# Performance work log

Measured on AMD Instinct MI355X. Metric: run time of the kernel, lower is better.

## Reference

```python
import jax, jax.numpy as jnp
import numpy as np

N = 50_000
E = 800_000
H = 128
EDGE_DIM = 1
NEG = 0.01  # leaky_relu slope used throughout AttentiveFP


def _lrelu(x):
    return jnp.where(x >= 0, x, NEG * x)


def _seg_softmax(logits, seg, num_segments):
    # numerically stable softmax over edges grouped by target segment
    m = jax.ops.segment_max(logits, seg, num_segments=num_segments)
    e = jnp.exp(logits - m[seg])
    s = jax.ops.segment_sum(e, seg, num_segments=num_segments)
    return e / s[seg]


def _gru(x, h, Wih, Whh, bih, bhh):
    # torch.nn.GRUCell: gates ordered r, z, n
    gi = x @ Wih.T + bih
    gh = h @ Whh.T + bhh
    ir, iz, inn = jnp.split(gi, 3, axis=-1)
    hr, hz, hn = jnp.split(gh, 3, axis=-1)
    r = jax.nn.sigmoid(ir + hr)
    z = jax.nn.sigmoid(iz + hz)
    n = jnp.tanh(inn + r * hn)
    return (1.0 - z) * n + z * h


def setup_inputs() -> dict:
    key = jax.random.key(0)
    ks = jax.random.split(key, 32)
    def rn(k, shape, s=0.1):
        return jax.random.normal(k, shape, dtype=jnp.float32) * s
    return {
        "node_attr": jax.random.normal(ks[0], (N, 1), dtype=jnp.float32),
        "edge_index": jax.random.randint(ks[1], (2, E), 0, N),
        "edge_attr": jax.random.normal(ks[2], (E, EDGE_DIM), dtype=jnp.float32),
        "W_lin1": rn(ks[3], (H, 1)), "b_lin1": rn(ks[4], (H,)),
        "gate_W1": rn(ks[5], (H, H + EDGE_DIM)), "gate_W2": rn(ks[6], (H, H)),
        "gate_att_l": rn(ks[7], (H,)), "gate_att_r": rn(ks[8], (H,)),
        "gate_b": rn(ks[9], (H,)),
        "gru1_Wih": rn(ks[10], (3 * H, H)), "gru1_Whh": rn(ks[11], (3 * H, H)),
        "gru1_bih": rn(ks[12], (3 * H,)), "gru1_bhh": rn(ks[13], (3 * H,)),
        "atom_W": rn(ks[14], (H, H)), "atom_att_src": rn(ks[15], (H,)),
        "atom_att_dst": rn(ks[16], (H,)), "atom_b": rn(ks[17], (H,)),
        "gru2_Wih": rn(ks[18], (3 * H, H)), "gru2_Whh": rn(ks[19], (3 * H, H)),
        "gru2_bih": rn(ks[20], (3 * H,)), "gru2_bhh": rn(ks[21], (3 * H,)),
        "mol_W": rn(ks[22], (H, H)), "mol_att_src": rn(ks[23], (H,)),
        "mol_att_dst": rn(ks[24], (H,)), "mol_b": rn(ks[25], (H,)),
        "grum_Wih": rn(ks[26], (3 * H, H)), "grum_Whh": rn(ks[27], (3 * H, H)),
        "grum_bih": rn(ks[28], (3 * H,)), "grum_bhh": rn(ks[29], (3 * H,)),
    }


def _forward(node_attr, edge_index, edge_attr, W_lin1, b_lin1, gate_W1, gate_W2,
             gate_att_l, gate_att_r, gate_b, gru1_Wih, gru1_Whh, gru1_bih, gru1_bhh,
             atom_W, atom_att_src, atom_att_dst, atom_b, gru2_Wih, gru2_Whh,
             gru2_bih, gru2_bhh, mol_W, mol_att_src, mol_att_dst, mol_b,
             grum_Wih, grum_Whh, grum_bih, grum_bhh):
    src, dst = edge_index[0], edge_index[1]  # j -> i (aggregate at dst)
    n = node_attr.shape[0]
    # lin1 + leaky_relu
    x = _lrelu(node_attr @ W_lin1.T + b_lin1)  # [N,H]
    # --- GATEConv (edge-featured attention) ---
    xj = _lrelu(jnp.concatenate([x[src], edge_attr], axis=-1) @ gate_W1.T)  # [E,H]
    alpha = _lrelu(xj @ gate_att_l + (x @ gate_att_r)[dst])  # [E]
    alpha = _seg_softmax(alpha, dst, n)
    h = jax.ops.segment_sum((x[src] @ gate_W2.T) * alpha[:, None], dst, num_segments=n) + gate_b
    h = jax.nn.elu(h)
    x = jax.nn.relu(_gru(h, x, gru1_Wih, gru1_Whh, gru1_bih, gru1_bhh))
    # --- GATConv layer (num_layers=2 -> one) ---
    xt = x @ atom_W.T  # [N,H]
    a = _lrelu((xt * atom_att_src).sum(-1)[src] + (xt * atom_att_dst).sum(-1)[dst])
    a = _seg_softmax(a, dst, n)
    h = jax.ops.segment_sum(xt[src] * a[:, None], dst, num_segments=n) + atom_b
    h = jax.nn.elu(h)
    x = jax.nn.relu(_gru(h, x, gru2_Wih, gru2_Whh, gru2_bih, gru2_bhh))
    # --- molecule embedding: batch = zeros -> single graph; num_timesteps=1 ---
    batch = jnp.zeros((n,), dtype=jnp.int32)
    out = jax.nn.relu(jax.ops.segment_sum(x, batch, num_segments=1))  # [1,H]
    xs = x @ mol_W.T          # node-side transform (shared lin)
    outs = out @ mol_W.T      # graph-side transform
    a = _lrelu((xs * mol_att_src).sum(-1) + (outs * mol_att_dst).sum(-1)[batch])
    a = _seg_softmax(a, batch, 1)
    h = jax.nn.elu(jax.ops.segment_sum(xs * a[:, None], batch, num_segments=1) + mol_b)
    out = jax.nn.relu(_gru(h, out, grum_Wih, grum_Whh, grum_bih, grum_bhh))
    return out  # [1, H] graph embedding (layer1 output, out_channels=hidden)


def reference(node_attr, edge_index, edge_attr, W_lin1, b_lin1, gate_W1, gate_W2,
              gate_att_l, gate_att_r, gate_b, gru1_Wih, gru1_Whh, gru1_bih, gru1_bhh,
              atom_W, atom_att_src, atom_att_dst, atom_b, gru2_Wih, gru2_Whh,
              gru2_bih, gru2_bhh, mol_W, mol_att_src, mol_att_dst, mol_b,
              grum_Wih, grum_Whh, grum_bih, grum_bhh):
    return _forward(node_attr, edge_index, edge_attr, W_lin1, b_lin1, gate_W1,
                    gate_W2, gate_att_l, gate_att_r, gate_b, gru1_Wih, gru1_Whh,
                    gru1_bih, gru1_bhh, atom_W, atom_att_src, atom_att_dst, atom_b,
                    gru2_Wih, gru2_Whh, gru2_bih, gru2_bhh, mol_W, mol_att_src,
                    mol_att_dst, mol_b, grum_Wih, grum_Whh, grum_bih, grum_bhh)
```

## Files before the change

### kernel.cpp

```cpp
#include <hip/hip_runtime.h>
#include <math.h>

#define H 128
#define NEGS 0.01f

typedef __attribute__((ext_vector_type(8))) short short8;
typedef __attribute__((ext_vector_type(4))) float f32x4;

__device__ __forceinline__ float lrelu(float x){ return x >= 0.f ? x : NEGS*x; }
__device__ __forceinline__ float eluf(float x){ return x > 0.f ? x : expf(x)-1.f; }
__device__ __forceinline__ float sigm(float x){ return 1.f/(1.f+expf(-x)); }
__device__ __forceinline__ float wred(float v){
  #pragma unroll
  for (int off = 32; off > 0; off >>= 1) v += __shfl_xor(v, off, 64);
  return v;
}
__device__ __forceinline__ float wredmax(float v){
  #pragma unroll
  for (int off = 32; off > 0; off >>= 1) v = fmaxf(v, __shfl_xor(v, off, 64));
  return v;
}
__device__ __forceinline__ unsigned fenc(float f){
  unsigned u = __float_as_uint(f);
  return (u & 0x80000000u) ? ~u : (u | 0x80000000u);
}
__device__ __forceinline__ float fdec(unsigned v){
  return __uint_as_float((v & 0x80000000u) ? (v ^ 0x80000000u) : ~v);
}
__device__ __forceinline__ unsigned short f2bf(float f){
  unsigned u = __float_as_uint(f);
  u += 0x7fffu + ((u >> 16) & 1u);
  return (unsigned short)(u >> 16);
}
__device__ __forceinline__ float bf2f(unsigned short h){
  return __uint_as_float(((unsigned)h) << 16);
}
__device__ __forceinline__ float rdlane(float v, int l){
  return __int_as_float(__builtin_amdgcn_readlane(__float_as_int(v), l));
}
__device__ __forceinline__ int rdlanei(int v, int l){
  return __builtin_amdgcn_readlane(v, l);
}

#define SMS 140

__global__ void k_castall(const float* __restrict__ gW1, const float* __restrict__ gW2,
                          const float* __restrict__ atomW, const float* __restrict__ molW,
                          const float* __restrict__ g1ih, const float* __restrict__ g1hh,
                          const float* __restrict__ g2ih, const float* __restrict__ g2hh,
                          unsigned short* __restrict__ dst){
  int idx = blockIdx.x*256 + threadIdx.x;
  const float* src; int ld = 128; int off;
  if      (idx <  16384){ src = gW1;  ld = 129; off = idx; }
  else if (idx <  32768){ src = gW2;  off = idx -  16384; }
  else if (idx <  49152){ src = atomW;off = idx -  32768; }
  else if (idx <  65536){ src = molW; off = idx -  49152; }
  else if (idx < 114688){ src = g1ih; off = idx -  65536; }
  else if (idx < 163840){ src = g1hh; off = idx - 114688; }
  else if (idx < 212992){ src = g2ih; off = idx - 163840; }
  else                  { src = g2hh; off = idx - 212992; }
  int r = off >> 7, c = off & 127;
  dst[idx] = f2bf(src[r*ld + c]);
}

__global__ void k_node_init_rd(const float* __restrict__ na, const float* __restrict__ wl,
                               const float* __restrict__ bl, const float* __restrict__ attr,
                               unsigned short* __restrict__ x, float* __restrict__ rdot, int n){
  int i = blockIdx.x*4 + (threadIdx.x >> 6);
  int lane = threadIdx.x & 63;
  if (i >= n) return;
  float nav = na[i];
  float v0 = lrelu(nav*wl[2*lane]   + bl[2*lane]);
  float v1 = lrelu(nav*wl[2*lane+1] + bl[2*lane+1]);
  ushort2 o; o.x = f2bf(v0); o.y = f2bf(v1);
  *(ushort2*)&x[(size_t)i*H + 2*lane] = o;
  float d = bf2f(o.x)*attr[2*lane] + bf2f(o.y)*attr[2*lane+1];
  d = wred(d);
  if (lane == 0) rdot[i] = d;
}

__global__ __launch_bounds__(256)
void k_gemm_mfma(const unsigned short* __restrict__ X, const unsigned short* __restrict__ Wbf,
                 unsigned short* __restrict__ Y, int n, int ldy, size_t ostride,
                 const float* __restrict__ v1, const float* __restrict__ v2,
                 float* __restrict__ o1, float* __restrict__ o2){
  __shared__ unsigned short sm[128*SMS];
  int w = threadIdx.x >> 6;
  int l = threadIdx.x & 63;
  int nb = blockIdx.x*128;
  int mbase = blockIdx.y*128;
  int row = l & 15;
  int kg  = l >> 4;
  f32x4 acc[2][8];
  #pragma unroll
  for (int f = 0; f < 2; ++f)
    #pragma unroll
    for (int c = 0; c < 8; ++c) acc[f][c] = (f32x4){0.f,0.f,0.f,0.f};
  int a0 = nb + w*16 + row;
  int a1 = nb + 64 + w*16 + row;
  bool v0 = (a0 < n), v1ok = (a1 < n);
  #pragma unroll
  for (int ks = 0; ks < 4; ++ks){
    int koff = ks*32 + kg*8;
    short8 A0 = v0  ? *(const short8*)&X[(size_t)a0*H + koff] : (short8){0,0,0,0,0,0,0,0};
    short8 A1 = v1ok? *(const short8*)&X[(size_t)a1*H + koff] : (short8){0,0,0,0,0,0,0,0};
    #pragma unroll
    for (int c = 0; c < 8; ++c){
      short8 b = *(const short8*)&Wbf[(size_t)(mbase + c*16 + row)*H + koff];
      acc[0][c] = __builtin_amdgcn_mfma_f32_16x16x32_bf16(A0, b, acc[0][c], 0, 0, 0);
      acc[1][c] = __builtin_amdgcn_mfma_f32_16x16x32_bf16(A1, b, acc[1][c], 0, 0, 0);
    }
  }
  #pragma unroll
  for (int f = 0; f < 2; ++f)
    #pragma unroll
    for (int c = 0; c < 8; ++c)
      #pragma unroll
      for (int r = 0; r < 4; ++r){
        int nl = f*64 + w*16 + kg*4 + r;
        sm[nl*SMS + c*16 + row] = f2bf(acc[f][c][r]);
      }
  if (v1){
    #pragma unroll
    for (int f = 0; f < 2; ++f)
      #pragma unroll
      for (int r = 0; r < 4; ++r){
        float p1 = 0.f, p2 = 0.f;
        #pragma unroll
        for (int c = 0; c < 8; ++c){
          p1 += acc[f][c][r]*v1[c*16 + row];
          if (v2) p2 += acc[f][c][r]*v2[c*16 + row];
        }
        #pragma unroll
        for (int off = 1; off < 16; off <<= 1){
          p1 += __shfl_xor(p1, off, 64);
          if (v2) p2 += __shfl_xor(p2, off, 64);
        }
        int i = nb + f*64 + w*16 + kg*4 + r;
        if (row == 0 && i < n){ o1[i] = p1; if (v2) o2[i] = p2; }
      }
  }
  __syncthreads();
  unsigned short* Yb = Y + (size_t)blockIdx.y*ostride;
  int t = threadIdx.x;
  #pragma unroll
  for (int p = 0; p < 16; ++p){
    int nl = p*8 + (t >> 5);
    int c4 = (t & 31)*4;
    int i = nb + nl;
    if (i < n) *(ushort4*)&Yb[(size_t)i*ldy + c4] = *(const ushort4*)&sm[nl*SMS + c4];
  }
}

__global__ __launch_bounds__(256)
void k_gemm_gru(const unsigned short* __restrict__ Xi, const unsigned short* __restrict__ Xh,
                const unsigned short* __restrict__ Wbf, unsigned short* __restrict__ gi,
                unsigned short* __restrict__ gh, int n){
  __shared__ unsigned short sm[128*SMS];
  int w = threadIdx.x >> 6;
  int l = threadIdx.x & 63;
  int nb = blockIdx.x*256;
  int y = blockIdx.y;
  const unsigned short* X = (y < 3) ? Xi : Xh;
  unsigned short* Y = (y < 3) ? gi : gh;
  int mbase = y*128;
  int cbase = (y < 3 ? y : y-3)*128;
  int row = l & 15;
  int kg  = l >> 4;
  f32x4 acc[4][8];
  #pragma unroll
  for (int f = 0; f < 4; ++f)
    #pragma unroll
    for (int c = 0; c < 8; ++c) acc[f][c] = (f32x4){0.f,0.f,0.f,0.f};
  int ai[4]; bool av[4];
  #pragma unroll
  for (int f = 0; f < 4; ++f){
    ai[f] = nb + f*64 + w*16 + row;
    av[f] = (ai[f] < n);
  }
  #pragma unroll
  for (int ks = 0; ks < 4; ++ks){
    int koff = ks*32 + kg*8;
    short8 A[4];
    #pragma unroll
    for (int f = 0; f < 4; ++f)
      A[f] = av[f] ? *(const short8*)&X[(size_t)ai[f]*H + koff] : (short8){0,0,0,0,0,0,0,0};
    #pragma unroll
    for (int c = 0; c < 8; ++c){
      short8 b = *(const short8*)&Wbf[(size_t)(mbase + c*16 + row)*H + koff];
      acc[0][c] = __builtin_amdgcn_mfma_f32_16x16x32_bf16(A[0], b, acc[0][c], 0, 0, 0);
      acc[1][c] = __builtin_amdgcn_mfma_f32_16x16x32_bf16(A[1], b, acc[1][c], 0, 0, 0);
      acc[2][c] = __builtin_amdgcn_mfma_f32_16x16x32_bf16(A[2], b, acc[2][c], 0, 0, 0);
      acc[3][c] = __builtin_amdgcn_mfma_f32_16x16x32_bf16(A[3], b, acc[3][c], 0, 0, 0);
    }
  }
  int t = threadIdx.x;
  #pragma unroll
  for (int half = 0; half < 2; ++half){
    if (half) __syncthreads();
    #pragma unroll
    for (int ff = 0; ff < 2; ++ff){
      int f = half*2 + ff;
      #pragma unroll
      for (int c = 0; c < 8; ++c)
        #pragma unroll
        for (int r = 0; r < 4; ++r){
          int nl = ff*64 + w*16 + kg*4 + r;
          sm[nl*SMS + c*16 + row] = f2bf(acc[f][c][r]);
        }
    }
    __syncthreads();
    #pragma unroll
    for (int p = 0; p < 16; ++p){
      int nl = p*8 + (t >> 5);
      int c4 = (t & 31)*4;
      int i = nb + half*128 + nl;
      if (i < n) *(ushort4*)&Y[(size_t)i*384 + cbase + c4] = *(const ushort4*)&sm[nl*SMS + c4];
    }
  }
}

__global__ void k_gru_combine(const unsigned short* __restrict__ gi, const unsigned short* __restrict__ gh,
                              const float* __restrict__ bih, const float* __restrict__ bhh,
                              unsigned short* __restrict__ x, int n){
  int idx = blockIdx.x*blockDim.x + threadIdx.x;
  if (idx >= n*64) return;
  int i = idx >> 6, t = (idx & 63)*2;
  const unsigned short* gir = gi + (size_t)i*384;
  const unsigned short* ghr = gh + (size_t)i*384;
  ushort2 uir = *(const ushort2*)&gir[t];
  ushort2 uiz = *(const ushort2*)&gir[t+128];
  ushort2 uin = *(const ushort2*)&gir[t+256];
  ushort2 uhr = *(const ushort2*)&ghr[t];
  ushort2 uhz = *(const ushort2*)&ghr[t+128];
  ushort2 uhn = *(const ushort2*)&ghr[t+256];
  ushort2 ux  = *(const ushort2*)&x[(size_t)i*H + t];
  float2 b_ir = *(const float2*)&bih[t], b_iz = *(const float2*)&bih[t+128], b_in = *(const float2*)&bih[t+256];
  float2 b_hr = *(const float2*)&bhh[t], b_hz = *(const float2*)&bhh[t+128], b_hn = *(const float2*)&bhh[t+256];
  ushort2 o;
  {
    float r = sigm(bf2f(uir.x)+b_ir.x + bf2f(uhr.x)+b_hr.x);
    float z = sigm(bf2f(uiz.x)+b_iz.x + bf2f(uhz.x)+b_hz.x);
    float nn = tanhf(bf2f(uin.x)+b_in.x + r*(bf2f(uhn.x)+b_hn.x));
    o.x = f2bf(fmaxf((1.f-z)*nn + z*bf2f(ux.x), 0.f));
  }
  {
    float r = sigm(bf2f(uir.y)+b_ir.y + bf2f(uhr.y)+b_hr.y);
    float z = sigm(bf2f(uiz.y)+b_iz.y + bf2f(uhz.y)+b_hz.y);
    float nn = tanhf(bf2f(uin.y)+b_in.y + r*(bf2f(uhn.y)+b_hn.y));
    o.y = f2bf(fmaxf((1.f-z)*nn + z*bf2f(ux.y), 0.f));
  }
  *(ushort2*)&x[(size_t)i*H + t] = o;
}

__global__ void k_hist(const int* __restrict__ key, int* __restrict__ deg, int ne){
  int e = blockIdx.x*blockDim.x + threadIdx.x;
  if (e < ne) atomicAdd(&deg[key[e]], 1);
}
__global__ void k_scan1(const int* __restrict__ deg, int* __restrict__ bsum, int n){
  __shared__ int sd[256];
  int i = blockIdx.x*256 + threadIdx.x;
  sd[threadIdx.x] = (i < n) ? deg[i] : 0;
  __syncthreads();
  for (int s = 128; s > 0; s >>= 1){
    if (threadIdx.x < s) sd[threadIdx.x] += sd[threadIdx.x+s];
    __syncthreads();
  }
  if (threadIdx.x == 0) bsum[blockIdx.x] = sd[0];
}
__global__ void k_scan2(int* __restrict__ bsum, int nb){
  __shared__ int sd[256];
  int t = threadIdx.x;
  int v = (t < nb) ? bsum[t] : 0;
  sd[t] = v;
  __syncthreads();
  for (int off = 1; off < 256; off <<= 1){
    int u = (t >= off) ? sd[t-off] : 0;
    __syncthreads();
    sd[t] += u;
    __syncthreads();
  }
  if (t < nb) bsum[t] = sd[t] - v;
}
__global__ void k_scan3(const int* __restrict__ deg, const int* __restrict__ boff,
                        int* __restrict__ rowptr, int* __restrict__ cursor, int n){
  __shared__ int sd[256];
  int t = threadIdx.x;
  int i = blockIdx.x*256 + t;
  int v = (i < n) ? deg[i] : 0;
  sd[t] = v;
  __syncthreads();
  for (int off = 1; off < 256; off <<= 1){
    int u = (t >= off) ? sd[t-off] : 0;
    __syncthreads();
    sd[t] += u;
    __syncthreads();
  }
  int excl = sd[t] - v + boff[blockIdx.x];
  if (i < n){
    rowptr[i] = excl; cursor[i] = excl;
    if (i == n-1) rowptr[n] = excl + v;
  }
}
__global__ void k_fill_dst(const int* __restrict__ src, const int* __restrict__ dst,
                           const float* __restrict__ ea, int* __restrict__ cursor,
                           int2* __restrict__ sea, int ne){
  int e = blockIdx.x*blockDim.x + threadIdx.x;
  if (e >= ne) return;
  int pos = atomicAdd(&cursor[dst[e]], 1);
  sea[pos] = make_int2(src[e], __float_as_int(ea[e]));
}

__global__ void k_pack_gate(const float* __restrict__ gateW1, float* __restrict__ w1col){
  int t = threadIdx.x;
  if (t < H) w1col[t] = gateW1[t*129 + 128];
}

__global__ __launch_bounds__(256)
void k_edge_logit_gate(const unsigned short* __restrict__ xW1, const float* __restrict__ w1col,
                       const float* __restrict__ attl, const int2* __restrict__ sea,
                       float* __restrict__ logit_s, int ne){
  int tid = threadIdx.x;
  int j = blockIdx.x*32 + (tid >> 3);
  int g = tid & 7;
  if (j >= ne) return;
  int2 se = sea[j];
  int s = se.x;
  float eav = __int_as_float(se.y);
  const unsigned short* xr = &xW1[(size_t)s*H + g*16];
  short8 r0 = *(const short8*)xr;
  short8 r1 = *(const short8*)(xr + 8);
  float acc = 0.f;
  #pragma unroll
  for (int kk = 0; kk < 8; ++kk)
    acc += lrelu(bf2f((unsigned short)r0[kk]) + eav*w1col[g*16 + kk]) * attl[g*16 + kk];
  #pragma unroll
  for (int kk = 0; kk < 8; ++kk)
    acc += lrelu(bf2f((unsigned short)r1[kk]) + eav*w1col[g*16 + 8 + kk]) * attl[g*16 + 8 + kk];
  #pragma unroll
  for (int off = 1; off < 8; off <<= 1) acc += __shfl_xor(acc, off, 64);
  if (g == 0) logit_s[j] = acc;
}

__global__ void k_node_agg(const int* __restrict__ rowptr, const int2* __restrict__ sea,
                           const float* __restrict__ logit_s, const float* __restrict__ rdot,
                           const unsigned short* __restrict__ val, const float* __restrict__ bias,
                           unsigned short* __restrict__ hbuf, int n){
  int i = blockIdx.x*4 + (threadIdx.x >> 6);
  int lane = threadIdx.x & 63;
  if (i >= n) return;
  int b = rowptr[i], e1 = rowptr[i+1];
  float rd = rdot[i];
  float m = -1e30f;
  for (int j = b+lane; j < e1; j += 64) m = fmaxf(m, lrelu(logit_s[j] + rd));
  m = wredmax(m);
  float s = 0.f, ax = 0.f, ay = 0.f;
  for (int c0 = b; c0 < e1; c0 += 64){
    int cnt = min(64, e1 - c0);
    float wv = 0.f; int snv = 0;
    if (lane < cnt){
      snv = sea[c0 + lane].x;
      wv = expf(lrelu(logit_s[c0 + lane] + rd) - m);
    }
    s += wred(wv);
    int j = 0;
    for (; j+8 <= cnt; j += 8){
      #pragma unroll
      for (int u = 0; u < 8; ++u){
        float wq = rdlane(wv, j+u);
        int sq = rdlanei(snv, j+u);
        ushort2 v = *(const ushort2*)&val[(size_t)sq*H + 2*lane];
        ax += bf2f(v.x)*wq; ay += bf2f(v.y)*wq;
      }
    }
    for (; j < cnt; ++j){
      float wq = rdlane(wv, j);
      int sq = rdlanei(snv, j);
      ushort2 v = *(const ushort2*)&val[(size_t)sq*H + 2*lane];
      ax += bf2f(v.x)*wq; ay += bf2f(v.y)*wq;
    }
  }
  float inv = (s > 0.f) ? 1.f/s : 0.f;
  ushort2 o;
  o.x = f2bf(eluf(bias[2*lane]   + ax*inv));
  o.y = f2bf(eluf(bias[2*lane+1] + ay*inv));
  *(ushort2*)&hbuf[(size_t)i*H + 2*lane] = o;
}

__global__ void k_node_agg_gat(const int* __restrict__ rowptr, const int2* __restrict__ sea,
                               const float* __restrict__ ssrc, const float* __restrict__ sdst,
                               const unsigned short* __restrict__ val, const float* __restrict__ bias,
                               unsigned short* __restrict__ hbuf, int n){
  int i = blockIdx.x*4 + (threadIdx.x >> 6);
  int lane = threadIdx.x & 63;
  if (i >= n) return;
  int b = rowptr[i], e1 = rowptr[i+1];
  float sdi = sdst[i];
  float m = -1e30f;
  for (int j = b+lane; j < e1; j += 64) m = fmaxf(m, lrelu(ssrc[sea[j].x] + sdi));
  m = wredmax(m);
  float s = 0.f, ax = 0.f, ay = 0.f;
  for (int c0 = b; c0 < e1; c0 += 64){
    int cnt = min(64, e1 - c0);
    float wv = 0.f; int snv = 0;
    if (lane < cnt){
      snv = sea[c0 + lane].x;
      wv = expf(lrelu(ssrc[snv] + sdi) - m);
    }
    s += wred(wv);
    int j = 0;
    for (; j+8 <= cnt; j += 8){
      #pragma unroll
      for (int u = 0; u < 8; ++u){
        float wq = rdlane(wv, j+u);
        int sq = rdlanei(snv, j+u);
        ushort2 v = *(const ushort2*)&val[(size_t)sq*H + 2*lane];
        ax += bf2f(v.x)*wq; ay += bf2f(v.y)*wq;
      }
    }
    for (; j < cnt; ++j){
      float wq = rdlane(wv, j);
      int sq = rdlanei(snv, j);
      ushort2 v = *(const ushort2*)&val[(size_t)sq*H + 2*lane];
      ax += bf2f(v.x)*wq; ay += bf2f(v.y)*wq;
    }
  }
  float inv = (s > 0.f) ? 1.f/s : 0.f;
  ushort2 o;
  o.x = f2bf(eluf(bias[2*lane]   + ax*inv));
  o.y = f2bf(eluf(bias[2*lane+1] + ay*inv));
  *(ushort2*)&hbuf[(size_t)i*H + 2*lane] = o;
}

__global__ void k_colsum(const unsigned short* __restrict__ x, float* __restrict__ outraw,
                         int n, int chunk){
  int t = threadIdx.x;
  int start = blockIdx.x*chunk;
  int end = min(start + chunk, n);
  float s0 = 0.f, s1 = 0.f;
  for (int i = start; i < end; ++i){
    ushort2 v = *(const ushort2*)&x[(size_t)i*H + 2*t];
    s0 += bf2f(v.x); s1 += bf2f(v.y);
  }
  if (start < end){ atomicAdd(&outraw[2*t], s0); atomicAdd(&outraw[2*t+1], s1); }
}
__global__ void k_mol_prep(const float* __restrict__ outraw, const float* __restrict__ molW,
                           const float* __restrict__ attdst, float* __restrict__ hidvec,
                           float* __restrict__ cdst){
  __shared__ float hs[128];
  __shared__ float red[128];
  int t = threadIdx.x;
  float hv = fmaxf(outraw[t], 0.f);
  hs[t] = hv; hidvec[t] = hv;
  __syncthreads();
  float o = 0.f;
  for (int k = 0; k < 128; ++k) o += hs[k]*molW[t*128+k];
  red[t] = o * attdst[t];
  __syncthreads();
  for (int s = 64; s > 0; s >>= 1){
    if (t < s) red[t] += red[t+s];
    __syncthreads();
  }
  if (t == 0) cdst[0] = red[0];
}
__global__ void k_mol_logit(float* __restrict__ a, const float* __restrict__ cdst,
                            unsigned* __restrict__ gmax, int n){
  int i = blockIdx.x*blockDim.x + threadIdx.x;
  int lane = threadIdx.x & 63;
  float l = -1e30f;
  if (i < n){
    l = lrelu(a[i] + cdst[0]);
    a[i] = l;
  }
  float mm = wredmax(l);
  if (lane == 0) atomicMax(gmax, fenc(mm));
}
__global__ void k_mol_exp(float* __restrict__ a, const unsigned* __restrict__ gmax,
                          float* __restrict__ gsum, int n){
  int i = blockIdx.x*blockDim.x + threadIdx.x;
  int lane = threadIdx.x & 63;
  float gm = fdec(gmax[0]);
  float ex = 0.f;
  if (i < n){ ex = expf(a[i] - gm); a[i] = ex; }
  float s = wred(ex);
  if (lane == 0) atomicAdd(gsum, s);
}
__global__ void k_mol_acc(const unsigned short* __restrict__ xs, const float* __restrict__ a,
                          float* __restrict__ num, int n, int chunk){
  int t = threadIdx.x;
  int start = blockIdx.x*chunk;
  int end = min(start + chunk, n);
  float s0 = 0.f, s1 = 0.f;
  for (int i = start; i < end; ++i){
    float ai = a[i];
    ushort2 v = *(const ushort2*)&xs[(size_t)i*H + 2*t];
    s0 += bf2f(v.x)*ai; s1 += bf2f(v.y)*ai;
  }
  if (start < end){ atomicAdd(&num[2*t], s0); atomicAdd(&num[2*t+1], s1); }
}
__global__ void k_mol_final(const float* __restrict__ num, const float* __restrict__ gsum,
                            const float* __restrict__ molb, const float* __restrict__ hidvec,
                            const float* __restrict__ Wih, const float* __restrict__ Whh,
                            const float* __restrict__ bih, const float* __restrict__ bhh,
                            float* __restrict__ out){
  __shared__ float hv[128], hd[128];
  int t = threadIdx.x;
  hv[t] = eluf(num[t]/gsum[0] + molb[t]);
  hd[t] = hidvec[t];
  __syncthreads();
  float gr = bih[t], gz = bih[t+128], gn = bih[t+256];
  float hr = bhh[t], hz = bhh[t+128], hn = bhh[t+256];
  for (int k = 0; k < 128; ++k){
    float h = hv[k], d = hd[k];
    gr += h*Wih[t*128+k];       gz += h*Wih[(t+128)*128+k]; gn += h*Wih[(t+256)*128+k];
    hr += d*Whh[t*128+k];       hz += d*Whh[(t+128)*128+k]; hn += d*Whh[(t+256)*128+k];
  }
  float r = sigm(gr+hr), z = sigm(gz+hz);
  float nn = tanhf(gn + r*hn);
  float o = (1.f-z)*nn + z*hd[t];
  out[t] = fmaxf(o, 0.f);
}

extern "C" void kernel_launch(void* const* d_in, const int* in_sizes, int n_in,
                              void* d_out, int out_size, void* d_ws, size_t ws_size,
                              hipStream_t stream){
  const float* node_attr = (const float*)d_in[0];
  const int*   eidx      = (const int*)d_in[1];
  const float* eattr     = (const float*)d_in[2];
  const float* W_lin1    = (const float*)d_in[3];
  const float* b_lin1    = (const float*)d_in[4];
  const float* gate_W1   = (const float*)d_in[5];
  const float* gate_W2   = (const float*)d_in[6];
  const float* gate_att_l= (const float*)d_in[7];
  const float* gate_att_r= (const float*)d_in[8];
  const float* gate_b    = (const float*)d_in[9];
  const float* g1_Wih    = (const float*)d_in[10];
  const float* g1_Whh    = (const float*)d_in[11];
  const float* g1_bih    = (const float*)d_in[12];
  const float* g1_bhh    = (const float*)d_in[13];
  const float* atom_W    = (const float*)d_in[14];
  const float* atom_as   = (const float*)d_in[15];
  const float* atom_ad   = (const float*)d_in[16];
  const float* atom_b    = (const float*)d_in[17];
  const float* g2_Wih    = (const float*)d_in[18];
  const float* g2_Whh    = (const float*)d_in[19];
  const float* g2_bih    = (const float*)d_in[20];
  const float* g2_bhh    = (const float*)d_in[21];
  const float* mol_W     = (const float*)d_in[22];
  const float* mol_as    = (const float*)d_in[23];
  const float* mol_ad    = (const float*)d_in[24];
  const float* mol_b     = (const float*)d_in[25];
  const float* gm_Wih    = (const float*)d_in[26];
  const float* gm_Whh    = (const float*)d_in[27];
  const float* gm_bih    = (const float*)d_in[28];
  const float* gm_bhh    = (const float*)d_in[29];

  const int n  = in_sizes[0];
  const int ne = in_sizes[1] / 2;
  const int* src = eidx;
  const int* dst = eidx + ne;

  const size_t NH = (size_t)n * H;
  unsigned short* us = (unsigned short*)d_ws;
  unsigned short* x_bf = us;
  unsigned short* t0   = us + NH;
  unsigned short* t1   = us + 2*NH;
  unsigned short* hb   = us + 3*NH;
  unsigned short* gi   = us + 4*NH;
  unsigned short* gh   = us + 7*NH;
  float* fb = (float*)(us + 10*NH);
  float* rdot = fb;
  float* ssrc = rdot + n;
  float* sdst = ssrc + n;
  float* logit_s = sdst + n;
  int* deg    = (int*)(logit_s + ne);
  int* cursor = deg + n;
  int* rowptr = cursor + n;
  int* bsum   = rowptr + n + 1;
  size_t ioff = (size_t)(bsum + 256 - (int*)d_ws);
  ioff = (ioff + 1) & ~(size_t)1;
  int2* sea  = (int2*)((int*)d_ws + ioff);
  float* outraw = (float*)(sea + ne);
  float* hidvec = outraw + 128;
  float* cdstp  = hidvec + 128;
  unsigned* gmax = (unsigned*)(cdstp + 1);
  float* gsum   = (float*)gmax + 1;
  float* numv   = gsum + 1;
  float* w1col  = numv + 128 + 1;
  unsigned short* wp = (unsigned short*)(w1col + 128);
  unsigned short* gW1bf  = wp;
  unsigned short* gW2bf  = gW1bf  + 128*H;
  unsigned short* atomWbf= gW2bf  + 128*H;
  unsigned short* molWbf = atomWbf+ 128*H;
  unsigned short* g1ihbf = molWbf + 128*H;
  unsigned short* g1hhbf = g1ihbf + 384*H;
  unsigned short* g2ihbf = g1hhbf + 384*H;
  unsigned short* g2hhbf = g2ihbf + 384*H;

  const int nb128      = (n + 127)/128;
  const int nb256      = (n + 255)/256;
  const int nwave4     = (n + 3)/4;
  const int e32_blocks = (ne + 31)/32;
  const int ethr       = (ne + 255)/256;
  const int nthr       = (n + 255)/256;
  const int nb         = (n + 255)/256;
  const int chunk      = (n + 255)/256;
  const int gru_blocks = (n*64 + 255)/256;

  k_castall<<<1024,256,0,stream>>>(gate_W1, gate_W2, atom_W, mol_W,
                                   g1_Wih, g1_Whh, g2_Wih, g2_Whh, wp);
  k_pack_gate<<<1,128,0,stream>>>(gate_W1, w1col);
  k_node_init_rd<<<nwave4,256,0,stream>>>(node_attr, W_lin1, b_lin1, gate_att_r, x_bf, rdot, n);
  hipMemsetAsync(deg, 0, (size_t)n*4, stream);
  k_hist<<<ethr,256,0,stream>>>(dst, deg, ne);
  k_scan1<<<nb,256,0,stream>>>(deg, bsum, n);
  k_scan2<<<1,256,0,stream>>>(bsum, nb);
  k_scan3<<<nb,256,0,stream>>>(deg, bsum, rowptr, cursor, n);
  k_fill_dst<<<ethr,256,0,stream>>>(src, dst, eattr, cursor, sea, ne);

  k_gemm_mfma<<<dim3(nb128,2),256,0,stream>>>(x_bf, gW1bf, t0, n, H, NH,
                                              nullptr, nullptr, nullptr, nullptr);
  k_edge_logit_gate<<<e32_blocks,256,0,stream>>>(t0, w1col, gate_att_l, sea, logit_s, ne);
  k_node_agg<<<nwave4,256,0,stream>>>(rowptr, sea, logit_s, rdot, t1, gate_b, hb, n);
  k_gemm_gru<<<dim3(nb256,6),256,0,stream>>>(hb, x_bf, g1ihbf, gi, gh, n);
  k_gru_combine<<<gru_blocks,256,0,stream>>>(gi, gh, g1_bih, g1_bhh, x_bf, n);

  k_gemm_mfma<<<dim3(nb128,1),256,0,stream>>>(x_bf, atomWbf, t0, n, H, 0,
                                              atom_as, atom_ad, ssrc, sdst);
  k_node_agg_gat<<<nwave4,256,0,stream>>>(rowptr, sea, ssrc, sdst, t0, atom_b, hb, n);
  k_gemm_gru<<<dim3(nb256,6),256,0,stream>>>(hb, x_bf, g2ihbf, gi, gh, n);
  k_gru_combine<<<gru_blocks,256,0,stream>>>(gi, gh, g2_bih, g2_bhh, x_bf, n);

  hipMemsetAsync(outraw, 0, 128*4, stream);
  hipMemsetAsync(gmax, 0, 4, stream);
  hipMemsetAsync(gsum, 0, 4, stream);
  hipMemsetAsync(numv, 0, 128*4, stream);
  k_colsum<<<256,64,0,stream>>>(x_bf, outraw, n, chunk);
  k_mol_prep<<<1,128,0,stream>>>(outraw, mol_W, mol_ad, hidvec, cdstp);
  k_gemm_mfma<<<dim3(nb128,1),256,0,stream>>>(x_bf, molWbf, t1, n, H, 0,
                                              mol_as, nullptr, rdot, nullptr);
  k_mol_logit<<<nthr,256,0,stream>>>(rdot, cdstp, gmax, n);
  k_mol_exp<<<nthr,256,0,stream>>>(rdot, gmax, gsum, n);
  k_mol_acc<<<256,64,0,stream>>>(t1, rdot, numv, n, chunk);
  k_mol_final<<<1,128,0,stream>>>(numv, gsum, mol_b, hidvec,
                                  gm_Wih, gm_Whh, gm_bih, gm_bhh, (float*)d_out);
}
```

Before: 616.3 us.

## Widen GEMM row tile to 256 and split wave into half-waves in aggregation

The MFMA GEMM now processes 256 rows per block instead of 128, reusing each loaded weight fragment across four A fragments and staging output through shared memory in two halves. The node aggregation kernels now have each half-wave handle a different edge, loading 8 bytes per lane with shuffles in place of readlane, so two neighbour rows are gathered per iteration, and reduce the halves at the end. This aims to cut redundant weight loads in the GEMM and raise memory-level parallelism in the gather. The cost is higher register pressure from 128 accumulator floats per lane, half as many GEMM blocks, and an extra cross-half reduction.

```diff
diff --git a/kernel.cpp b/kernel.cpp
--- a/kernel.cpp
+++ b/kernel.cpp
@@ -34,12 +34,6 @@
 }
 __device__ __forceinline__ float bf2f(unsigned short h){
   return __uint_as_float(((unsigned)h) << 16);
-}
-__device__ __forceinline__ float rdlane(float v, int l){
-  return __int_as_float(__builtin_amdgcn_readlane(__float_as_int(v), l));
-}
-__device__ __forceinline__ int rdlanei(int v, int l){
-  return __builtin_amdgcn_readlane(v, l);
 }
 
 #define SMS 140
@@ -87,42 +81,40 @@
   __shared__ unsigned short sm[128*SMS];
   int w = threadIdx.x >> 6;
   int l = threadIdx.x & 63;
-  int nb = blockIdx.x*128;
+  int nb = blockIdx.x*256;
   int mbase = blockIdx.y*128;
   int row = l & 15;
   int kg  = l >> 4;
-  f32x4 acc[2][8];
-  #pragma unroll
-  for (int f = 0; f < 2; ++f)
+  f32x4 acc[4][8];
+  #pragma unroll
+  for (int f = 0; f < 4; ++f)
     #pragma unroll
     for (int c = 0; c < 8; ++c) acc[f][c] = (f32x4){0.f,0.f,0.f,0.f};
-  int a0 = nb + w*16 + row;
-  int a1 = nb + 64 + w*16 + row;
-  bool v0 = (a0 < n), v1ok = (a1 < n);
+  int ai[4]; bool av[4];
+  #pragma unroll
+  for (int f = 0; f < 4; ++f){
+    ai[f] = nb + f*64 + w*16 + row;
+    av[f] = (ai[f] < n);
+  }
   #pragma unroll
   for (int ks = 0; ks < 4; ++ks){
     int koff = ks*32 + kg*8;
-    short8 A0 = v0  ? *(const short8*)&X[(size_t)a0*H + koff] : (short8){0,0,0,0,0,0,0,0};
-    short8 A1 = v1ok? *(const short8*)&X[(size_t)a1*H + koff] : (short8){0,0,0,0,0,0,0,0};
+    short8 A[4];
+    #pragma unroll
+    for (int f = 0; f < 4; ++f)
+      A[f] = av[f] ? *(const short8*)&X[(size_t)ai[f]*H + koff] : (short8){0,0,0,0,0,0,0,0};
     #pragma unroll
     for (int c = 0; c < 8; ++c){
       short8 b = *(const short8*)&Wbf[(size_t)(mbase + c*16 + row)*H + koff];
-      acc[0][c] = __builtin_amdgcn_mfma_f32_16x16x32_bf16(A0, b, acc[0][c], 0, 0, 0);
-      acc[1][c] = __builtin_amdgcn_mfma_f32_16x16x32_bf16(A1, b, acc[1][c], 0, 0, 0);
-    }
-  }
-  #pragma unroll
-  for (int f = 0; f < 2; ++f)
-    #pragma unroll
-    for (int c = 0; c < 8; ++c)
-      #pragma unroll
-      for (int r = 0; r < 4; ++r){
-        int nl = f*64 + w*16 + kg*4 + r;
-        sm[nl*SMS + c*16 + row] = f2bf(acc[f][c][r]);
-      }
+      acc[0][c] = __builtin_amdgcn_mfma_f32_16x16x32_bf16(A[0], b, acc[0][c], 0, 0, 0);
+      acc[1][c] = __builtin_amdgcn_mfma_f32_16x16x32_bf16(A[1], b, acc[1][c], 0, 0, 0);
+      acc[2][c] = __builtin_amdgcn_mfma_f32_16x16x32_bf16(A[2], b, acc[2][c], 0, 0, 0);
+      acc[3][c] = __builtin_amdgcn_mfma_f32_16x16x32_bf16(A[3], b, acc[3][c], 0, 0, 0);
+    }
+  }
   if (v1){
     #pragma unroll
-    for (int f = 0; f < 2; ++f)
+    for (int f = 0; f < 4; ++f)
       #pragma unroll
       for (int r = 0; r < 4; ++r){
         float p1 = 0.f, p2 = 0.f;
@@ -140,15 +132,30 @@
         if (row == 0 && i < n){ o1[i] = p1; if (v2) o2[i] = p2; }
       }
   }
-  __syncthreads();
   unsigned short* Yb = Y + (size_t)blockIdx.y*ostride;
   int t = threadIdx.x;
   #pragma unroll
-  for (int p = 0; p < 16; ++p){
-    int nl = p*8 + (t >> 5);
-    int c4 = (t & 31)*4;
-    int i = nb + nl;
-    if (i < n) *(ushort4*)&Yb[(size_t)i*ldy + c4] = *(const ushort4*)&sm[nl*SMS + c4];
+  for (int half = 0; half < 2; ++half){
+    if (half) __syncthreads();
+    #pragma unroll
+    for (int ff = 0; ff < 2; ++ff){
+      int f = half*2 + ff;
+      #pragma unroll
+      for (int c = 0; c < 8; ++c)
+        #pragma unroll
+        for (int r = 0; r < 4; ++r){
+          int nl = ff*64 + w*16 + kg*4 + r;
+          sm[nl*SMS + c*16 + row] = f2bf(acc[f][c][r]);
+        }
+    }
+    __syncthreads();
+    #pragma unroll
+    for (int p = 0; p < 16; ++p){
+      int nl = p*8 + (t >> 5);
+      int c4 = (t & 31)*4;
+      int i = nb + half*128 + nl;
+      if (i < n) *(ushort4*)&Yb[(size_t)i*ldy + c4] = *(const ushort4*)&sm[nl*SMS + c4];
+    }
   }
 }
 
@@ -348,13 +355,16 @@
                            unsigned short* __restrict__ hbuf, int n){
   int i = blockIdx.x*4 + (threadIdx.x >> 6);
   int lane = threadIdx.x & 63;
+  int hl = lane >> 5;
+  int cl = lane & 31;
   if (i >= n) return;
   int b = rowptr[i], e1 = rowptr[i+1];
   float rd = rdot[i];
   float m = -1e30f;
   for (int j = b+lane; j < e1; j += 64) m = fmaxf(m, lrelu(logit_s[j] + rd));
   m = wredmax(m);
-  float s = 0.f, ax = 0.f, ay = 0.f;
+  float s = 0.f;
+  float a0=0.f, a1=0.f, a2=0.f, a3=0.f;
   for (int c0 = b; c0 < e1; c0 += 64){
     int cnt = min(64, e1 - c0);
     float wv = 0.f; int snv = 0;
@@ -364,27 +374,41 @@
     }
     s += wred(wv);
     int j = 0;
-    for (; j+8 <= cnt; j += 8){
+    for (; j+16 <= cnt; j += 16){
       #pragma unroll
       for (int u = 0; u < 8; ++u){
-        float wq = rdlane(wv, j+u);
-        int sq = rdlanei(snv, j+u);
-        ushort2 v = *(const ushort2*)&val[(size_t)sq*H + 2*lane];
-        ax += bf2f(v.x)*wq; ay += bf2f(v.y)*wq;
+        int jj = j + 2*u + hl;
+        float wq = __shfl(wv, jj, 64);
+        int sq = __shfl(snv, jj, 64);
+        ushort4 v = *(const ushort4*)&val[(size_t)sq*H + 4*cl];
+        a0 += bf2f(v.x)*wq; a1 += bf2f(v.y)*wq; a2 += bf2f(v.z)*wq; a3 += bf2f(v.w)*wq;
       }
     }
-    for (; j < cnt; ++j){
-      float wq = rdlane(wv, j);
-      int sq = rdlanei(snv, j);
-      ushort2 v = *(const ushort2*)&val[(size_t)sq*H + 2*lane];
-      ax += bf2f(v.x)*wq; ay += bf2f(v.y)*wq;
-    }
-  }
+    for (; j < cnt; j += 2){
+      int jj = j + hl;
+      int jjc = jj < 63 ? jj : 63;
+      float wq = __shfl(wv, jjc, 64);
+      int sq = __shfl(snv, jjc, 64);
+      if (jj < cnt){
+        ushort4 v = *(const ushort4*)&val[(size_t)sq*H + 4*cl];
+        a0 += bf2f(v.x)*wq; a1 += bf2f(v.y)*wq; a2 += bf2f(v.z)*wq; a3 += bf2f(v.w)*wq;
+      }
+    }
+  }
+  a0 += __shfl_xor(a0, 32, 64);
+  a1 += __shfl_xor(a1, 32, 64);
+  a2 += __shfl_xor(a2, 32, 64);
+  a3 += __shfl_xor(a3, 32, 64);
   float inv = (s > 0.f) ? 1.f/s : 0.f;
-  ushort2 o;
-  o.x = f2bf(eluf(bias[2*lane]   + ax*inv));
-  o.y = f2bf(eluf(bias[2*lane+1] + ay*inv));
-  *(ushort2*)&hbuf[(size_t)i*H + 2*lane] = o;
+  if (hl == 0){
+    float4 bb = *(const float4*)&bias[4*cl];
+    ushort4 o;
+    o.x = f2bf(eluf(bb.x + a0*inv));
+    o.y = f2bf(eluf(bb.y + a1*inv));
+    o.z = f2bf(eluf(bb.z + a2*inv));
+    o.w = f2bf(eluf(bb.w + a3*inv));
+    *(ushort4*)&hbuf[(size_t)i*H + 4*cl] = o;
+  }
 }
 
 __global__ void k_node_agg_gat(const int* __restrict__ rowptr, const int2* __restrict__ sea,
@@ -393,13 +417,16 @@
                                unsigned short* __restrict__ hbuf, int n){
   int i = blockIdx.x*4 + (threadIdx.x >> 6);
   int lane = threadIdx.x & 63;
+  int hl = lane >> 5;
+  int cl = lane & 31;
   if (i >= n) return;
   int b = rowptr[i], e1 = rowptr[i+1];
   float sdi = sdst[i];
   float m = -1e30f;
   for (int j = b+lane; j < e1; j += 64) m = fmaxf(m, lrelu(ssrc[sea[j].x] + sdi));
   m = wredmax(m);
-  float s = 0.f, ax = 0.f, ay = 0.f;
+  float s = 0.f;
+  float a0=0.f, a1=0.f, a2=0.f, a3=0.f;
   for (int c0 = b; c0 < e1; c0 += 64){
     int cnt = min(64, e1 - c0);
     float wv = 0.f; int snv = 0;
@@ -409,27 +436,41 @@
     }
     s += wred(wv);
     int j = 0;
-    for (; j+8 <= cnt; j += 8){
+    for (; j+16 <= cnt; j += 16){
       #pragma unroll
       for (int u = 0; u < 8; ++u){
-        float wq = rdlane(wv, j+u);
-        int sq = rdlanei(snv, j+u);
-        ushort2 v = *(const ushort2*)&val[(size_t)sq*H + 2*lane];
-        ax += bf2f(v.x)*wq; ay += bf2f(v.y)*wq;
+        int jj = j + 2*u + hl;
+        float wq = __shfl(wv, jj, 64);
+        int sq = __shfl(snv, jj, 64);
+        ushort4 v = *(const ushort4*)&val[(size_t)sq*H + 4*cl];
+        a0 += bf2f(v.x)*wq; a1 += bf2f(v.y)*wq; a2 += bf2f(v.z)*wq; a3 += bf2f(v.w)*wq;
       }
     }
-    for (; j < cnt; ++j){
-      float wq = rdlane(wv, j);
-      int sq = rdlanei(snv, j);
-      ushort2 v = *(const ushort2*)&val[(size_t)sq*H + 2*lane];
-      ax += bf2f(v.x)*wq; ay += bf2f(v.y)*wq;
-    }
-  }
+    for (; j < cnt; j += 2){
+      int jj = j + hl;
+      int jjc = jj < 63 ? jj : 63;
+      float wq = __shfl(wv, jjc, 64);
+      int sq = __shfl(snv, jjc, 64);
+      if (jj < cnt){
+        ushort4 v = *(const ushort4*)&val[(size_t)sq*H + 4*cl];
+        a0 += bf2f(v.x)*wq; a1 += bf2f(v.y)*wq; a2 += bf2f(v.z)*wq; a3 += bf2f(v.w)*wq;
+      }
+    }
+  }
+  a0 += __shfl_xor(a0, 32, 64);
+  a1 += __shfl_xor(a1, 32, 64);
+  a2 += __shfl_xor(a2, 32, 64);
+  a3 += __shfl_xor(a3, 32, 64);
   float inv = (s > 0.f) ? 1.f/s : 0.f;
-  ushort2 o;
-  o.x = f2bf(eluf(bias[2*lane]   + ax*inv));
-  o.y = f2bf(eluf(bias[2*lane+1] + ay*inv));
-  *(ushort2*)&hbuf[(size_t)i*H + 2*lane] = o;
+  if (hl == 0){
+    float4 bb = *(const float4*)&bias[4*cl];
+    ushort4 o;
+    o.x = f2bf(eluf(bb.x + a0*inv));
+    o.y = f2bf(eluf(bb.y + a1*inv));
+    o.z = f2bf(eluf(bb.z + a2*inv));
+    o.w = f2bf(eluf(bb.w + a3*inv));
+    *(ushort4*)&hbuf[(size_t)i*H + 4*cl] = o;
+  }
 }
 
 __global__ void k_colsum(const unsigned short* __restrict__ x, float* __restrict__ outraw,
@@ -597,7 +638,6 @@
   unsigned short* g2ihbf = g1hhbf + 384*H;
   unsigned short* g2hhbf = g2ihbf + 384*H;
 
-  const int nb128      = (n + 127)/128;
   const int nb256      = (n + 255)/256;
   const int nwave4     = (n + 3)/4;
   const int e32_blocks = (ne + 31)/32;
@@ -618,14 +658,14 @@
   k_scan3<<<nb,256,0,stream>>>(deg, bsum, rowptr, cursor, n);
   k_fill_dst<<<ethr,256,0,stream>>>(src, dst, eattr, cursor, sea, ne);
 
-  k_gemm_mfma<<<dim3(nb128,2),256,0,stream>>>(x_bf, gW1bf, t0, n, H, NH,
+  k_gemm_mfma<<<dim3(nb256,2),256,0,stream>>>(x_bf, gW1bf, t0, n, H, NH,
                                               nullptr, nullptr, nullptr, nullptr);
   k_edge_logit_gate<<<e32_blocks,256,0,stream>>>(t0, w1col, gate_att_l, sea, logit_s, ne);
   k_node_agg<<<nwave4,256,0,stream>>>(rowptr, sea, logit_s, rdot, t1, gate_b, hb, n);
   k_gemm_gru<<<dim3(nb256,6),256,0,stream>>>(hb, x_bf, g1ihbf, gi, gh, n);
   k_gru_combine<<<gru_blocks,256,0,stream>>>(gi, gh, g1_bih, g1_bhh, x_bf, n);
 
-  k_gemm_mfma<<<dim3(nb128,1),256,0,stream>>>(x_bf, atomWbf, t0, n, H, 0,
+  k_gemm_mfma<<<dim3(nb256,1),256,0,stream>>>(x_bf, atomWbf, t0, n, H, 0,
                                               atom_as, atom_ad, ssrc, sdst);
   k_node_agg_gat<<<nwave4,256,0,stream>>>(rowptr, sea, ssrc, sdst, t0, atom_b, hb, n);
   k_gemm_gru<<<dim3(nb256,6),256,0,stream>>>(hb, x_bf, g2ihbf, gi, gh, n);
@@ -637,7 +677,7 @@
   hipMemsetAsync(numv, 0, 128*4, stream);
   k_colsum<<<256,64,0,stream>>>(x_bf, outraw, n, chunk);
   k_mol_prep<<<1,128,0,stream>>>(outraw, mol_W, mol_ad, hidvec, cdstp);
-  k_gemm_mfma<<<dim3(nb128,1),256,0,stream>>>(x_bf, molWbf, t1, n, H, 0,
+  k_gemm_mfma<<<dim3(nb256,1),256,0,stream>>>(x_bf, molWbf, t1, n, H, 0,
                                               mol_as, nullptr, rdot, nullptr);
   k_mol_logit<<<nthr,256,0,stream>>>(rdot, cdstp, gmax, n);
   k_mol_exp<<<nthr,256,0,stream>>>(rdot, gmax, gsum, n);
```

Result: slower. 642.4 us (+4.2%).
